# Kernel optimization log

Hardware: AMD Instinct MI355X
Metric: run time of the kernel (lower is better)

Reference implementation:

```python
import jax, jax.numpy as jnp
import numpy as np

B, N, T, D, M, HOPS = 32, 300, 12, 64, 16, 2

def setup_inputs() -> dict:
    key = jax.random.key(0)
    ks = jax.random.split(key, 12)
    inp = {
        "X": jax.random.normal(ks[0], (B, D, N, T), dtype=jnp.float32),
        "timeEmbedding": jax.random.normal(ks[1], (B, N, T, D), dtype=jnp.float32),
        "adjW": jax.random.normal(ks[2], (N, D), dtype=jnp.float32) * (1.0 / np.sqrt(D)),
        "adjB": jnp.zeros((N,), dtype=jnp.float32),
        "trainW1": jax.random.normal(ks[3], (N, M), dtype=jnp.float32) * 0.1,
        "trainW2": jax.random.normal(ks[4], (M, D * D), dtype=jnp.float32) * 0.1,
        "alpha1": jax.random.normal(ks[5], (N, M), dtype=jnp.float32) * 0.1,
        "alpha2": jax.random.normal(ks[6], (M, N), dtype=jnp.float32) * 0.1,
        "beta1": jax.random.normal(ks[7], (N, M), dtype=jnp.float32) * 0.1,
        "beta2": jax.random.normal(ks[8], (M, N), dtype=jnp.float32) * 0.1,
        "gcnW": jax.random.normal(ks[9], (D, D * (HOPS + 1)), dtype=jnp.float32) * (1.0 / np.sqrt(D * (HOPS + 1))),
        "gcnB": jnp.zeros((D,), dtype=jnp.float32),
    }
    return inp

def reference(X, timeEmbedding, adjW, adjB, trainW1, trainW2, alpha1, alpha2, beta1, beta2, gcnW, gcnB):
    # timeEmbedding: [B,N,T,D] -> [B,T,N,D]
    te = jnp.transpose(timeEmbedding, (0, 2, 1, 3))
    # learned adjacency: A[b,t,n,k]
    A = jnp.sin(jnp.einsum('btnd,kd->btnk', te, adjW) + adjB)  # Linear(dmodel->N)
    A = (alpha1 @ alpha2) * A            # elementwise scale by [N,N], broadcast over b,t
    A = jax.nn.relu(A + beta1 @ beta2)
    # X: [B,D,N,T] -> [B,T,N,D]
    Xp = jnp.transpose(X, (0, 3, 2, 1))
    # per-node weight matrices [N,D,D]
    W = (trainW1 @ trainW2).reshape(N, D, D)
    Hs = [Xp]
    Hb = Xp
    for _ in range(HOPS):
        Hnow = jnp.einsum('btnk,btkd->btnd', A, Hb)      # adjacency aggregation
        Hnow = jnp.einsum('btnk,nkd->btnd', Hnow, W)     # per-node distinct matmul
        pre = Xp + Hnow
        Hnow = jax.nn.sigmoid(pre) * jnp.tanh(pre)        # gated residual
        Hs.append(Hnow)
        Hb = Hnow
    H = jnp.concatenate(Hs, axis=3)                       # [B,T,N,D*(hops+1)]
    Hout = jnp.einsum('btnf,df->btnd', H, gcnW) + gcnB    # gcnLinear (dropout = identity in eval)
    return jnp.transpose(Hout, (0, 3, 2, 1))              # [B,D,N,T]
```

## Files before the change

kernel.cpp:

```cpp
#include <hip/hip_runtime.h>

#define Nq 300
#define Tq 12
#define Dq 64
#define Mq 16
#define BTq 384
#define DDq (Dq*Dq)
#define Fq (Dq*3)
#define NP 320

typedef short bf8_t __attribute__((ext_vector_type(8)));
typedef float f4_t  __attribute__((ext_vector_type(4)));

__device__ __forceinline__ unsigned short f2bf(float f) {
    unsigned u = __float_as_uint(f);
    u = (u + 0x7FFFu + ((u >> 16) & 1u)) >> 16;
    return (unsigned short)u;
}
__device__ __forceinline__ float bf2f(unsigned short u) {
    return __uint_as_float((unsigned)u << 16);
}
__device__ __forceinline__ float4 ld4(const float* p) { return *(const float4*)p; }

__device__ __forceinline__ bf8_t pack8(float4 a, float4 b) {
    bf8_t r;
    r[0] = (short)f2bf(a.x); r[1] = (short)f2bf(a.y);
    r[2] = (short)f2bf(a.z); r[3] = (short)f2bf(a.w);
    r[4] = (short)f2bf(b.x); r[5] = (short)f2bf(b.y);
    r[6] = (short)f2bf(b.z); r[7] = (short)f2bf(b.w);
    return r;
}

__device__ __forceinline__ float gatef(float p) {
    float pc = fminf(fmaxf(p, -30.f), 30.f);
    float sig = 1.f / (1.f + __expf(-pc));
    float e2  = __expf(2.f * pc);
    float th  = (e2 - 1.f) / (e2 + 1.f);
    return sig * th;
}

__global__ void kprep_ab(const float* __restrict__ a1, const float* __restrict__ a2,
                         const float* __restrict__ b1, const float* __restrict__ b2,
                         unsigned* __restrict__ ABp) {
    int e = blockIdx.x * 256 + threadIdx.x;
    if (e >= Nq * Nq) return;
    int n = e / Nq, k = e - n * Nq;
    float sa = 0.f, sb = 0.f;
    #pragma unroll
    for (int m = 0; m < Mq; ++m) {
        sa = fmaf(a1[n*Mq+m], a2[m*Nq+k], sa);
        sb = fmaf(b1[n*Mq+m], b2[m*Nq+k], sb);
    }
    ABp[e] = ((unsigned)f2bf(sb) << 16) | (unsigned)f2bf(sa);
}

__global__ void __launch_bounds__(256) kprep_W(const float* __restrict__ w1,
                                               const float* __restrict__ w2,
                                               unsigned short* __restrict__ Wt) {
    __shared__ float sT[64 * 65];
    __shared__ float sw1[Mq];
    const int n = blockIdx.x;
    const int tid = threadIdx.x;
    if (tid < Mq) sw1[tid] = w1[n*Mq + tid];
    __syncthreads();
    for (int i = tid; i < DDq; i += 256) {
        int k = i >> 6, d = i & 63;
        float s = 0.f;
        #pragma unroll
        for (int m = 0; m < Mq; ++m) s = fmaf(sw1[m], w2[m*DDq + i], s);
        sT[d*65 + k] = s;
    }
    __syncthreads();
    for (int i = tid; i < DDq; i += 256) {
        int d = i >> 6, k = i & 63;
        Wt[(size_t)n*DDq + i] = f2bf(sT[d*65 + k]);
    }
}

__global__ void kprep_adjW(const float* __restrict__ adjW, unsigned short* __restrict__ adjWb) {
    int e = blockIdx.x * 256 + threadIdx.x;
    if (e >= 304 * 64) return;
    int k = e >> 6, d = e & 63;
    adjWb[e] = (k < Nq) ? f2bf(adjW[k*Dq + d]) : (unsigned short)0;
}

__global__ void __launch_bounds__(256) ktr_te(const float* __restrict__ te,
                                              unsigned short* __restrict__ te_b) {
    int i = blockIdx.x * 256 + threadIdx.x;
    int q = i & 15;
    int rem = i >> 4;
    int t = rem % Tq;
    int rem2 = rem / Tq;
    int n = rem2 % Nq;
    int b = rem2 / Nq;
    float4 v = ld4(&te[(((size_t)b*Nq + n)*Tq + t)*Dq + q*4]);
    ushort4 o;
    o.x = f2bf(v.x); o.y = f2bf(v.y); o.z = f2bf(v.z); o.w = f2bf(v.w);
    *(ushort4*)&te_b[(((size_t)(b*Tq + t))*Nq + n)*Dq + q*4] = o;
}

__global__ void __launch_bounds__(256) ktr_x(const float* __restrict__ X,
                                             unsigned short* __restrict__ Xp_t,
                                             unsigned short* __restrict__ Xp_nb) {
    __shared__ unsigned short sT[64 * 308];
    const int b = blockIdx.x / 12, tile = blockIdx.x % 12;
    const int n0 = tile * 25;
    const int tid = threadIdx.x;
    for (int i = tid; i < 64 * 300; i += 256) {
        int d = i / 300, j = i - d * 300;
        sT[d*308 + j] = f2bf(X[(size_t)(b*64 + d)*3600 + n0*12 + j]);
    }
    __syncthreads();
    for (int wi = tid; wi < 12 * 64 * 25; wi += 256) {
        int nl = wi % 25, rem = wi / 25;
        int d = rem % 64, t = rem / 64;
        Xp_t[((size_t)(b*Tq + t)*64 + d)*NP + n0 + nl] = sT[d*308 + nl*12 + t];
    }
    if (tile == 11) {
        for (int wi = tid; wi < 12 * 64 * 20; wi += 256) {
            int e = wi % 20, rem = wi / 20;
            int d = rem % 64, t = rem / 64;
            Xp_t[((size_t)(b*Tq + t)*64 + d)*NP + 300 + e] = 0;
        }
    }
    for (int wi = tid; wi < 25 * 12 * 64; wi += 256) {
        int d = wi & 63, rem = wi >> 6;
        int t = rem % 12, nl = rem / 12;
        Xp_nb[((size_t)(n0 + nl)*BTq + b*Tq + t)*64 + d] = sT[d*308 + nl*12 + t];
    }
}

__global__ void __launch_bounds__(256) ktr2(const unsigned short* __restrict__ Hnb,
                                            unsigned short* __restrict__ Ht) {
    __shared__ unsigned short sT[64 * 308];
    const int bt = blockIdx.x;
    const int tid = threadIdx.x;
    for (int i = tid; i < 300 * 64; i += 256) {
        int n = i >> 6, d = i & 63;
        sT[d*308 + n] = Hnb[((size_t)n*BTq + bt)*64 + d];
    }
    __syncthreads();
    for (int wi = tid; wi < 64 * 80; wi += 256) {
        int kq = wi % 80, d = wi / 80;
        ushort4 o;
        int k = kq * 4;
        o.x = (k+0 < Nq) ? sT[d*308 + k+0] : (unsigned short)0;
        o.y = (k+1 < Nq) ? sT[d*308 + k+1] : (unsigned short)0;
        o.z = (k+2 < Nq) ? sT[d*308 + k+2] : (unsigned short)0;
        o.w = (k+3 < Nq) ? sT[d*308 + k+3] : (unsigned short)0;
        *(ushort4*)&Ht[((size_t)bt*64 + d)*NP + k] = o;
    }
}

__global__ void __launch_bounds__(256, 3) kfuse(
    const unsigned short* __restrict__ te_b,
    const unsigned short* __restrict__ adjWb,
    const float* __restrict__ adjB,
    const unsigned* __restrict__ ABp,
    const unsigned short* __restrict__ Hb_t,
    unsigned short* __restrict__ Hout_nb)
{
    __shared__ unsigned short sPl[80 * 72];
    const int bt = blockIdx.x >> 2, qi = blockIdx.x & 3;
    const int nbase = qi * 80;
    const int tid = threadIdx.x;
    const int w = tid >> 6, lane = tid & 63, quad = lane >> 4, l16 = lane & 15;
    const int dcol = w*16 + l16;

    bf8_t ta0[5], ta1[5];
    #pragma unroll
    for (int rt = 0; rt < 5; ++rt) {
        int nr = nbase + rt*16 + l16; if (nr > Nq-1) nr = Nq-1;
        const unsigned short* r = te_b + ((size_t)bt*Nq + nr)*64;
        ta0[rt] = *(const bf8_t*)(r + quad*8);
        ta1[rt] = *(const bf8_t*)(r + 32 + quad*8);
    }
    f4_t accO[5];
    #pragma unroll
    for (int rt = 0; rt < 5; ++rt) accO[rt] = (f4_t){0.f, 0.f, 0.f, 0.f};

    for (int c = 0; c < 5; ++c) {
        const int cbase = c * 64;
        const int kglob = cbase + w*16 + l16;
        const int kc = (kglob > Nq-1) ? Nq-1 : kglob;
        const float bias = adjB[kc];
        const unsigned short* ar = adjWb + kc*64;
        bf8_t kb0 = *(const bf8_t*)(ar + quad*8);
        bf8_t kb1 = *(const bf8_t*)(ar + 32 + quad*8);
        #pragma unroll
        for (int rt = 0; rt < 5; ++rt) {
            f4_t p = {0.f, 0.f, 0.f, 0.f};
            p = __builtin_amdgcn_mfma_f32_16x16x32_bf16(ta0[rt], kb0, p, 0, 0, 0);
            p = __builtin_amdgcn_mfma_f32_16x16x32_bf16(ta1[rt], kb1, p, 0, 0, 0);
            #pragma unroll
            for (int reg = 0; reg < 4; ++reg) {
                int nl = rt*16 + quad*4 + reg;
                int ncp = nbase + nl; if (ncp > Nq-1) ncp = Nq-1;
                unsigned ab = ABp[ncp*Nq + kc];
                float alo = __uint_as_float(ab << 16);
                float ahi = __uint_as_float(ab & 0xFFFF0000u);
                float sv = __sinf(p[reg] + bias);
                float a = fmaf(alo, sv, ahi);
                a = fmaxf(a, 0.f);
                if (kglob > Nq-1) a = 0.f;
                sPl[nl*72 + w*16 + l16] = f2bf(a);
            }
        }
        __syncthreads();
        const unsigned short* hr = Hb_t + ((size_t)bt*64 + dcol)*NP + cbase;
        bf8_t v0 = *(const bf8_t*)(hr + quad*8);
        bf8_t v1 = *(const bf8_t*)(hr + 32 + quad*8);
        #pragma unroll
        for (int rt = 0; rt < 5; ++rt) {
            bf8_t p0 = *(const bf8_t*)&sPl[(rt*16 + l16)*72 + quad*8];
            bf8_t p1 = *(const bf8_t*)&sPl[(rt*16 + l16)*72 + 32 + quad*8];
            accO[rt] = __builtin_amdgcn_mfma_f32_16x16x32_bf16(p0, v0, accO[rt], 0, 0, 0);
            accO[rt] = __builtin_amdgcn_mfma_f32_16x16x32_bf16(p1, v1, accO[rt], 0, 0, 0);
        }
        __syncthreads();
    }
    #pragma unroll
    for (int rt = 0; rt < 5; ++rt) {
        #pragma unroll
        for (int reg = 0; reg < 4; ++reg) {
            int ng = nbase + rt*16 + quad*4 + reg;
            if (ng < Nq)
                Hout_nb[((size_t)ng*BTq + bt)*64 + dcol] = f2bf(accO[rt][reg]);
        }
    }
}

__global__ void __launch_bounds__(256) kmm(
    const unsigned short* __restrict__ Hagg_nb,
    const unsigned short* __restrict__ Xp_nb,
    const unsigned short* __restrict__ Wt,
    unsigned short* __restrict__ Hout_nb)
{
    const int n = blockIdx.x >> 2, qi = blockIdx.x & 3;
    const int bt0 = qi * 96;
    const int tid = threadIdx.x;
    const int w = tid >> 6, lane = tid & 63, quad = lane >> 4, l16 = lane & 15;
    const int dcol = w*16 + l16;
    const unsigned short* wn = Wt + (size_t)n * DDq + dcol*64;
    bf8_t v0 = *(const bf8_t*)(wn + quad*8);
    bf8_t v1 = *(const bf8_t*)(wn + 32 + quad*8);
    f4_t acc[6];
    #pragma unroll
    for (int rt = 0; rt < 6; ++rt) acc[rt] = (f4_t){0.f, 0.f, 0.f, 0.f};
    #pragma unroll
    for (int rt = 0; rt < 6; ++rt) {
        int r = bt0 + rt*16 + l16;
        const unsigned short* row = Hagg_nb + ((size_t)n*BTq + r)*64;
        bf8_t a0 = *(const bf8_t*)(row + quad*8);
        bf8_t a1 = *(const bf8_t*)(row + 32 + quad*8);
        acc[rt] = __builtin_amdgcn_mfma_f32_16x16x32_bf16(a0, v0, acc[rt], 0, 0, 0);
        acc[rt] = __builtin_amdgcn_mfma_f32_16x16x32_bf16(a1, v1, acc[rt], 0, 0, 0);
    }
    __syncthreads();
    #pragma unroll
    for (int rt = 0; rt < 6; ++rt) {
        #pragma unroll
        for (int reg = 0; reg < 4; ++reg) {
            int r = bt0 + rt*16 + quad*4 + reg;
            size_t idx = ((size_t)n*BTq + r)*64 + dcol;
            float xp = bf2f(Xp_nb[idx]);
            Hout_nb[idx] = f2bf(gatef(xp + acc[rt][reg]));
        }
    }
}

__global__ void __launch_bounds__(256) kgcn(
    const unsigned short* __restrict__ Xp_nb, const unsigned short* __restrict__ H1_nb,
    const unsigned short* __restrict__ H2_nb, const float* __restrict__ gcnW,
    const float* __restrict__ gcnB, float* __restrict__ out)
{
    const int b = blockIdx.x / 19, tile = blockIdx.x % 19;
    const int n0 = tile * 16;
    const int rows = (tile == 18) ? 144 : 192;
    const int tid = threadIdx.x;
    const int w = tid >> 6, lane = tid & 63, quad = lane >> 4, l16 = lane & 15;
    const int dcol = w*16 + l16;
    const float bias = gcnB[dcol];
    f4_t acc[12];
    #pragma unroll
    for (int rt = 0; rt < 12; ++rt) acc[rt] = (f4_t){0.f, 0.f, 0.f, 0.f};
    const unsigned short* bufs[3] = {Xp_nb, H1_nb, H2_nb};
    #pragma unroll
    for (int c = 0; c < 3; ++c) {
        const unsigned short* buf = bufs[c];
        const float* gwr = gcnW + (size_t)dcol*Fq + c*Dq;
        bf8_t v0 = pack8(ld4(gwr + quad*8),      ld4(gwr + quad*8 + 4));
        bf8_t v1 = pack8(ld4(gwr + 32 + quad*8), ld4(gwr + 36 + quad*8));
        #pragma unroll
        for (int rt = 0; rt < 12; ++rt) {
            int r = rt*16 + l16;
            int nl = r / 12, t = r - nl*12;
            int n = n0 + nl; if (n > Nq-1) n = Nq-1;
            const unsigned short* row = buf + ((size_t)n*BTq + b*Tq + t)*64;
            bf8_t a0 = *(const bf8_t*)(row + quad*8);
            bf8_t a1 = *(const bf8_t*)(row + 32 + quad*8);
            acc[rt] = __builtin_amdgcn_mfma_f32_16x16x32_bf16(a0, v0, acc[rt], 0, 0, 0);
            acc[rt] = __builtin_amdgcn_mfma_f32_16x16x32_bf16(a1, v1, acc[rt], 0, 0, 0);
        }
    }
    float* outd = out + (size_t)(b*Dq + dcol)*3600 + n0*12;
    #pragma unroll
    for (int rt = 0; rt < 12; ++rt) {
        if (rt*16 < rows) {
            int r0 = rt*16 + quad*4;
            float4 o = make_float4(acc[rt][0] + bias, acc[rt][1] + bias,
                                   acc[rt][2] + bias, acc[rt][3] + bias);
            *(float4*)&outd[r0] = o;
        }
    }
}

extern "C" void kernel_launch(void* const* d_in, const int* in_sizes, int n_in,
                              void* d_out, int out_size, void* d_ws, size_t ws_size,
                              hipStream_t stream) {
    (void)in_sizes; (void)n_in; (void)out_size; (void)ws_size;
    const float* X    = (const float*)d_in[0];
    const float* te   = (const float*)d_in[1];
    const float* adjW = (const float*)d_in[2];
    const float* adjB = (const float*)d_in[3];
    const float* w1   = (const float*)d_in[4];
    const float* w2   = (const float*)d_in[5];
    const float* a1   = (const float*)d_in[6];
    const float* a2   = (const float*)d_in[7];
    const float* b1   = (const float*)d_in[8];
    const float* b2   = (const float*)d_in[9];
    const float* gW   = (const float*)d_in[10];
    const float* gB   = (const float*)d_in[11];
    float* out = (float*)d_out;

    char* ws = (char*)d_ws;
    unsigned*       ABp    = (unsigned*)      (ws);
    unsigned short* adjWb  = (unsigned short*)(ws + 360064);
    unsigned short* Wt     = (unsigned short*)(ws + 398976);
    unsigned short* te_b   = (unsigned short*)(ws + 2856576);
    unsigned short* Xp_t   = (unsigned short*)(ws + 17602176);
    unsigned short* Xp_nb  = (unsigned short*)(ws + 33330816);
    unsigned short* Hagg   = (unsigned short*)(ws + 48076416);
    unsigned short* H1_nb  = (unsigned short*)(ws + 62822016);
    unsigned short* H1_t   = (unsigned short*)(ws + 77567616);

    hipLaunchKernelGGL(kprep_ab,   dim3(352),  dim3(256), 0, stream, a1, a2, b1, b2, ABp);
    hipLaunchKernelGGL(kprep_W,    dim3(300),  dim3(256), 0, stream, w1, w2, Wt);
    hipLaunchKernelGGL(kprep_adjW, dim3(76),   dim3(256), 0, stream, adjW, adjWb);
    hipLaunchKernelGGL(ktr_te,     dim3(7200), dim3(256), 0, stream, te, te_b);
    hipLaunchKernelGGL(ktr_x,      dim3(384),  dim3(256), 0, stream, X, Xp_t, Xp_nb);
    hipLaunchKernelGGL(kfuse, dim3(1536), dim3(256), 0, stream, te_b, adjWb, adjB, ABp, Xp_t, Hagg);
    hipLaunchKernelGGL(kmm,   dim3(1200), dim3(256), 0, stream, Hagg, Xp_nb, Wt, H1_nb);
    hipLaunchKernelGGL(ktr2,  dim3(384),  dim3(256), 0, stream, H1_nb, H1_t);
    hipLaunchKernelGGL(kfuse, dim3(1536), dim3(256), 0, stream, te_b, adjWb, adjB, ABp, H1_t, Hagg);
    hipLaunchKernelGGL(kmm,   dim3(1200), dim3(256), 0, stream, Hagg, Xp_nb, Wt, Hagg);
    hipLaunchKernelGGL(kgcn,  dim3(608), dim3(256), 0, stream, Xp_nb, H1_nb, Hagg, gW, gB, out);
}
```

Measured before the change: 330.3 us.

## Fuse time-embedding conversion into kfuse and pre-tile adjacency scale table

Drops the separate ktr_te transpose/convert pass, so kfuse reads fp32 time embeddings directly and packs them to bf16 in registers. The alpha/beta product table is now laid out in the exact MFMA fragment order, and the bias and adjW arrays are padded, which turns the scattered per-element loads into one uint4 load per tile and removes the bounds clamps. The MFMA operand order is swapped so each lane writes four contiguous bf16 values to LDS. The LDS tile is double-buffered to drop one barrier per chunk. In exchange, kfuse reads and converts the fp32 embeddings on both hops instead of reading the bf16 copy, and the launch-bounds occupancy hint is removed.

```diff
diff --git a/kernel.cpp b/kernel.cpp
--- a/kernel.cpp
+++ b/kernel.cpp
@@ -39,19 +39,28 @@
     return sig * th;
 }
 
-__global__ void kprep_ab(const float* __restrict__ a1, const float* __restrict__ a2,
-                         const float* __restrict__ b1, const float* __restrict__ b2,
-                         unsigned* __restrict__ ABp) {
-    int e = blockIdx.x * 256 + threadIdx.x;
-    if (e >= Nq * Nq) return;
-    int n = e / Nq, k = e - n * Nq;
-    float sa = 0.f, sb = 0.f;
-    #pragma unroll
-    for (int m = 0; m < Mq; ++m) {
-        sa = fmaf(a1[n*Mq+m], a2[m*Nq+k], sa);
-        sb = fmaf(b1[n*Mq+m], b2[m*Nq+k], sb);
-    }
-    ABp[e] = ((unsigned)f2bf(sb) << 16) | (unsigned)f2bf(sa);
+__global__ void kprep_abt(const float* __restrict__ a1, const float* __restrict__ a2,
+                          const float* __restrict__ b1, const float* __restrict__ b2,
+                          unsigned* __restrict__ ABt) {
+    const int tile = blockIdx.x;
+    const int tid  = threadIdx.x;
+    const int reg = tid & 3, lane = tid >> 2;
+    const int nt = tile % 5;  int r1 = tile / 5;
+    const int w  = r1 % 4;    int r2 = r1 / 4;
+    const int c  = r2 % 5;    const int qi = r2 / 5;
+    const int n = qi*80 + nt*16 + (lane & 15);
+    const int k = c*64 + w*16 + (lane >> 4)*4 + reg;
+    unsigned outv = 0u;
+    if (n < Nq && k < Nq) {
+        float sa = 0.f, sb = 0.f;
+        #pragma unroll
+        for (int m = 0; m < Mq; ++m) {
+            sa = fmaf(a1[n*Mq+m], a2[m*Nq+k], sa);
+            sb = fmaf(b1[n*Mq+m], b2[m*Nq+k], sb);
+        }
+        outv = ((unsigned)f2bf(sb) << 16) | (unsigned)f2bf(sa);
+    }
+    ABt[tile*256 + tid] = outv;
 }
 
 __global__ void __launch_bounds__(256) kprep_W(const float* __restrict__ w1,
@@ -77,26 +86,14 @@
     }
 }
 
-__global__ void kprep_adjW(const float* __restrict__ adjW, unsigned short* __restrict__ adjWb) {
+__global__ void kprep_adjW(const float* __restrict__ adjW, const float* __restrict__ adjB,
+                           unsigned short* __restrict__ adjWb, float* __restrict__ adjBp) {
     int e = blockIdx.x * 256 + threadIdx.x;
-    if (e >= 304 * 64) return;
-    int k = e >> 6, d = e & 63;
-    adjWb[e] = (k < Nq) ? f2bf(adjW[k*Dq + d]) : (unsigned short)0;
-}
-
-__global__ void __launch_bounds__(256) ktr_te(const float* __restrict__ te,
-                                              unsigned short* __restrict__ te_b) {
-    int i = blockIdx.x * 256 + threadIdx.x;
-    int q = i & 15;
-    int rem = i >> 4;
-    int t = rem % Tq;
-    int rem2 = rem / Tq;
-    int n = rem2 % Nq;
-    int b = rem2 / Nq;
-    float4 v = ld4(&te[(((size_t)b*Nq + n)*Tq + t)*Dq + q*4]);
-    ushort4 o;
-    o.x = f2bf(v.x); o.y = f2bf(v.y); o.z = f2bf(v.z); o.w = f2bf(v.w);
-    *(ushort4*)&te_b[(((size_t)(b*Tq + t))*Nq + n)*Dq + q*4] = o;
+    if (e < NP * 64) {
+        int k = e >> 6, d = e & 63;
+        adjWb[e] = (k < Nq) ? f2bf(adjW[k*Dq + d]) : (unsigned short)0;
+    }
+    if (e < NP) adjBp[e] = (e < Nq) ? adjB[e] : 0.f;
 }
 
 __global__ void __launch_bounds__(256) ktr_x(const float* __restrict__ X,
@@ -152,28 +149,29 @@
     }
 }
 
-__global__ void __launch_bounds__(256, 3) kfuse(
-    const unsigned short* __restrict__ te_b,
+__global__ void __launch_bounds__(256) kfuse(
+    const float* __restrict__ te,
     const unsigned short* __restrict__ adjWb,
-    const float* __restrict__ adjB,
-    const unsigned* __restrict__ ABp,
+    const float* __restrict__ adjBp,
+    const unsigned* __restrict__ ABt,
     const unsigned short* __restrict__ Hb_t,
     unsigned short* __restrict__ Hout_nb)
 {
-    __shared__ unsigned short sPl[80 * 72];
+    __shared__ unsigned short sPl[2][80 * 72];
     const int bt = blockIdx.x >> 2, qi = blockIdx.x & 3;
+    const int b = bt / Tq, t = bt - b * Tq;
     const int nbase = qi * 80;
     const int tid = threadIdx.x;
     const int w = tid >> 6, lane = tid & 63, quad = lane >> 4, l16 = lane & 15;
     const int dcol = w*16 + l16;
 
-    bf8_t ta0[5], ta1[5];
-    #pragma unroll
-    for (int rt = 0; rt < 5; ++rt) {
-        int nr = nbase + rt*16 + l16; if (nr > Nq-1) nr = Nq-1;
-        const unsigned short* r = te_b + ((size_t)bt*Nq + nr)*64;
-        ta0[rt] = *(const bf8_t*)(r + quad*8);
-        ta1[rt] = *(const bf8_t*)(r + 32 + quad*8);
+    bf8_t tb0[5], tb1[5];
+    #pragma unroll
+    for (int nt = 0; nt < 5; ++nt) {
+        int n = nbase + nt*16 + l16; if (n > Nq-1) n = Nq-1;
+        const float* ter = te + (((size_t)b*Nq + n)*Tq + t)*Dq;
+        tb0[nt] = pack8(ld4(ter + quad*8),      ld4(ter + quad*8 + 4));
+        tb1[nt] = pack8(ld4(ter + 32 + quad*8), ld4(ter + 36 + quad*8));
     }
     f4_t accO[5];
     #pragma unroll
@@ -181,30 +179,40 @@
 
     for (int c = 0; c < 5; ++c) {
         const int cbase = c * 64;
-        const int kglob = cbase + w*16 + l16;
-        const int kc = (kglob > Nq-1) ? Nq-1 : kglob;
-        const float bias = adjB[kc];
-        const unsigned short* ar = adjWb + kc*64;
-        bf8_t kb0 = *(const bf8_t*)(ar + quad*8);
-        bf8_t kb1 = *(const bf8_t*)(ar + 32 + quad*8);
-        #pragma unroll
-        for (int rt = 0; rt < 5; ++rt) {
+        const unsigned short* ar = adjWb + (cbase + w*16 + l16)*64;
+        bf8_t ka0 = *(const bf8_t*)(ar + quad*8);
+        bf8_t ka1 = *(const bf8_t*)(ar + 32 + quad*8);
+        float4 bias4 = ld4(adjBp + cbase + w*16 + quad*4);
+        const unsigned* abbase = ABt + ((((size_t)qi*5 + c)*4 + w)*5)*256 + lane*4;
+        unsigned short* sp = sPl[c & 1];
+        #pragma unroll
+        for (int nt = 0; nt < 5; ++nt) {
             f4_t p = {0.f, 0.f, 0.f, 0.f};
-            p = __builtin_amdgcn_mfma_f32_16x16x32_bf16(ta0[rt], kb0, p, 0, 0, 0);
-            p = __builtin_amdgcn_mfma_f32_16x16x32_bf16(ta1[rt], kb1, p, 0, 0, 0);
-            #pragma unroll
-            for (int reg = 0; reg < 4; ++reg) {
-                int nl = rt*16 + quad*4 + reg;
-                int ncp = nbase + nl; if (ncp > Nq-1) ncp = Nq-1;
-                unsigned ab = ABp[ncp*Nq + kc];
-                float alo = __uint_as_float(ab << 16);
-                float ahi = __uint_as_float(ab & 0xFFFF0000u);
-                float sv = __sinf(p[reg] + bias);
-                float a = fmaf(alo, sv, ahi);
-                a = fmaxf(a, 0.f);
-                if (kglob > Nq-1) a = 0.f;
-                sPl[nl*72 + w*16 + l16] = f2bf(a);
+            p = __builtin_amdgcn_mfma_f32_16x16x32_bf16(ka0, tb0[nt], p, 0, 0, 0);
+            p = __builtin_amdgcn_mfma_f32_16x16x32_bf16(ka1, tb1[nt], p, 0, 0, 0);
+            uint4 ab = *(const uint4*)(abbase + nt*256);
+            ushort4 o4;
+            {
+                float sv = __sinf(p[0] + bias4.x);
+                o4.x = f2bf(fmaxf(fmaf(__uint_as_float(ab.x << 16), sv,
+                                       __uint_as_float(ab.x & 0xFFFF0000u)), 0.f));
             }
+            {
+                float sv = __sinf(p[1] + bias4.y);
+                o4.y = f2bf(fmaxf(fmaf(__uint_as_float(ab.y << 16), sv,
+                                       __uint_as_float(ab.y & 0xFFFF0000u)), 0.f));
+            }
+            {
+                float sv = __sinf(p[2] + bias4.z);
+                o4.z = f2bf(fmaxf(fmaf(__uint_as_float(ab.z << 16), sv,
+                                       __uint_as_float(ab.z & 0xFFFF0000u)), 0.f));
+            }
+            {
+                float sv = __sinf(p[3] + bias4.w);
+                o4.w = f2bf(fmaxf(fmaf(__uint_as_float(ab.w << 16), sv,
+                                       __uint_as_float(ab.w & 0xFFFF0000u)), 0.f));
+            }
+            *(ushort4*)&sp[(nt*16 + l16)*72 + w*16 + quad*4] = o4;
         }
         __syncthreads();
         const unsigned short* hr = Hb_t + ((size_t)bt*64 + dcol)*NP + cbase;
@@ -212,12 +220,11 @@
         bf8_t v1 = *(const bf8_t*)(hr + 32 + quad*8);
         #pragma unroll
         for (int rt = 0; rt < 5; ++rt) {
-            bf8_t p0 = *(const bf8_t*)&sPl[(rt*16 + l16)*72 + quad*8];
-            bf8_t p1 = *(const bf8_t*)&sPl[(rt*16 + l16)*72 + 32 + quad*8];
+            bf8_t p0 = *(const bf8_t*)&sp[(rt*16 + l16)*72 + quad*8];
+            bf8_t p1 = *(const bf8_t*)&sp[(rt*16 + l16)*72 + 32 + quad*8];
             accO[rt] = __builtin_amdgcn_mfma_f32_16x16x32_bf16(p0, v0, accO[rt], 0, 0, 0);
             accO[rt] = __builtin_amdgcn_mfma_f32_16x16x32_bf16(p1, v1, accO[rt], 0, 0, 0);
         }
-        __syncthreads();
     }
     #pragma unroll
     for (int rt = 0; rt < 5; ++rt) {
@@ -334,25 +341,24 @@
     float* out = (float*)d_out;
 
     char* ws = (char*)d_ws;
-    unsigned*       ABp    = (unsigned*)      (ws);
-    unsigned short* adjWb  = (unsigned short*)(ws + 360064);
-    unsigned short* Wt     = (unsigned short*)(ws + 398976);
-    unsigned short* te_b   = (unsigned short*)(ws + 2856576);
-    unsigned short* Xp_t   = (unsigned short*)(ws + 17602176);
-    unsigned short* Xp_nb  = (unsigned short*)(ws + 33330816);
-    unsigned short* Hagg   = (unsigned short*)(ws + 48076416);
-    unsigned short* H1_nb  = (unsigned short*)(ws + 62822016);
-    unsigned short* H1_t   = (unsigned short*)(ws + 77567616);
-
-    hipLaunchKernelGGL(kprep_ab,   dim3(352),  dim3(256), 0, stream, a1, a2, b1, b2, ABp);
-    hipLaunchKernelGGL(kprep_W,    dim3(300),  dim3(256), 0, stream, w1, w2, Wt);
-    hipLaunchKernelGGL(kprep_adjW, dim3(76),   dim3(256), 0, stream, adjW, adjWb);
-    hipLaunchKernelGGL(ktr_te,     dim3(7200), dim3(256), 0, stream, te, te_b);
-    hipLaunchKernelGGL(ktr_x,      dim3(384),  dim3(256), 0, stream, X, Xp_t, Xp_nb);
-    hipLaunchKernelGGL(kfuse, dim3(1536), dim3(256), 0, stream, te_b, adjWb, adjB, ABp, Xp_t, Hagg);
+    unsigned*       ABt    = (unsigned*)      (ws);
+    unsigned short* adjWb  = (unsigned short*)(ws + 409600);
+    float*          adjBp  = (float*)         (ws + 450560);
+    unsigned short* Wt     = (unsigned short*)(ws + 451840);
+    unsigned short* Xp_t   = (unsigned short*)(ws + 2909440);
+    unsigned short* Xp_nb  = (unsigned short*)(ws + 18638080);
+    unsigned short* Hagg   = (unsigned short*)(ws + 33383680);
+    unsigned short* H1_nb  = (unsigned short*)(ws + 48129280);
+    unsigned short* H1_t   = (unsigned short*)(ws + 62874880);
+
+    hipLaunchKernelGGL(kprep_abt,  dim3(400), dim3(256), 0, stream, a1, a2, b1, b2, ABt);
+    hipLaunchKernelGGL(kprep_W,    dim3(300), dim3(256), 0, stream, w1, w2, Wt);
+    hipLaunchKernelGGL(kprep_adjW, dim3(80),  dim3(256), 0, stream, adjW, adjB, adjWb, adjBp);
+    hipLaunchKernelGGL(ktr_x,      dim3(384), dim3(256), 0, stream, X, Xp_t, Xp_nb);
+    hipLaunchKernelGGL(kfuse, dim3(1536), dim3(256), 0, stream, te, adjWb, adjBp, ABt, Xp_t, Hagg);
     hipLaunchKernelGGL(kmm,   dim3(1200), dim3(256), 0, stream, Hagg, Xp_nb, Wt, H1_nb);
     hipLaunchKernelGGL(ktr2,  dim3(384),  dim3(256), 0, stream, H1_nb, H1_t);
-    hipLaunchKernelGGL(kfuse, dim3(1536), dim3(256), 0, stream, te_b, adjWb, adjB, ABp, H1_t, Hagg);
+    hipLaunchKernelGGL(kfuse, dim3(1536), dim3(256), 0, stream, te, adjWb, adjBp, ABt, H1_t, Hagg);
     hipLaunchKernelGGL(kmm,   dim3(1200), dim3(256), 0, stream, Hagg, Xp_nb, Wt, Hagg);
     hipLaunchKernelGGL(kgcn,  dim3(608), dim3(256), 0, stream, Xp_nb, H1_nb, Hagg, gW, gB, out);
 }
```

After: 327.9 us. About the same (-0.7%).
